# Optimization experiments

Hardware: AMD Instinct MI355X
Metric: run time of the kernel (lower is better)

The kernel has to match this reference:

```python
import jax, jax.numpy as jnp
import numpy as np

B = 131072   # batch rows in the (pooled) sparse tensor
C = 512      # conv_out4
J = 7        # jnt_dim
H = 512      # linear_out
TAU_MAX = 1.0  # undefined global in source; torque cap, taken as 1.0
EPS = 1e-5


def layer_norm(x, g, b):
    m = jnp.mean(x, axis=-1, keepdims=True)
    v = jnp.var(x, axis=-1, keepdims=True)
    return (x - m) * jax.lax.rsqrt(v + EPS) * g + b


def setup_inputs() -> dict:
    key = jax.random.key(0)
    ks = jax.random.split(key, 6)
    return {
        "features": jax.random.normal(ks[0], (B, C), dtype=jnp.float32),
        "coords": jax.random.randint(ks[1], (B,), 0, B),  # batch indices (col 0 of ME coords)
        "jnt_pos": jax.random.normal(ks[2], (B, J), dtype=jnp.float32),
        "jnt_goal": jax.random.normal(ks[3], (B, J), dtype=jnp.float32),
        "ln1_g": jnp.ones((C,), jnp.float32),
        "ln1_b": jnp.zeros((C,), jnp.float32),
        "W1": jax.random.normal(ks[4], (C + 2 * J, H), dtype=jnp.float32) / np.sqrt(C + 2 * J),
        "b1": jnp.zeros((H,), jnp.float32),
        "ln2_g": jnp.ones((H,), jnp.float32),
        "ln2_b": jnp.zeros((H,), jnp.float32),
        "W2": jax.random.normal(ks[5], (H, J), dtype=jnp.float32) / np.sqrt(H),
        "b2": jnp.zeros((J,), jnp.float32),
    }


def reference(features, coords, jnt_pos, jnt_goal,
              ln1_g, ln1_b, W1, b1, ln2_g, ln2_b, W2, b2):
    # to_dense_tnsr: y = zeros_like(features); for c in coords: y[c] = features[c]
    # vectorized: single gather + scatter (duplicate writes carry identical values)
    y = jnp.zeros_like(features).at[coords].set(features[coords])
    # norm = LayerNorm(512) -> SELU   (dropout in eval mode: identity)
    x = jax.nn.selu(layer_norm(y, ln1_g, ln1_b))
    # cat((jnt_pos, jnt_goal, x), dim=1)
    x = jnp.concatenate([jnt_pos, jnt_goal, x], axis=1)  # [B, 2J+C]
    # linear = Linear -> LayerNorm -> SELU
    x = jax.nn.selu(layer_norm(x @ W1 + b1, ln2_g, ln2_b))
    # out = Linear -> Tanh, scaled by tau_max
    return jnp.tanh(x @ W2 + b2) * TAU_MAX
```

## Files before the change

kernel.cpp:

```cpp
#include <hip/hip_runtime.h>

#define B_ROWS   131072
#define MTILE    64
#define KCHUNKS  17
#define LDA      552
#define W1T_OFF  ((size_t)B_ROWS * 4)

typedef _Float16 f16x8 __attribute__((ext_vector_type(8)));
typedef float    f32x4 __attribute__((ext_vector_type(4)));

__device__ inline unsigned short f2h(float f) {
  _Float16 h = (_Float16)f;
  return __builtin_bit_cast(unsigned short, h);
}
__device__ inline float selu_f(float x) {
  const float lam = 1.0507009873554805f, alp = 1.6732632423543772f;
  return x > 0.f ? lam * x : lam * alp * (__expf(x) - 1.f);
}

__global__ void scatter_mask(const int* __restrict__ coords,
                             unsigned int* __restrict__ mask) {
  int i = blockIdx.x * 256 + threadIdx.x;
  mask[coords[i]] = 1u;
}

__global__ void build_w1f(const float* __restrict__ W1,
                          unsigned short* __restrict__ W1f) {
  int fragIdx = blockIdx.x;
  int tid  = threadIdx.x;
  int ni   = fragIdx & 3;
  int c    = (fragIdx >> 2) % 17;
  int wq   = fragIdx / 68;
  int lane = tid >> 3, e = tid & 7;
  int n = wq * 64 + ni * 16 + (lane & 15);
  int k = c * 32 + (lane >> 4) * 8 + e;
  float v = 0.f;
  if (k < 512)       v = W1[(size_t)(k + 14) * 512 + n];
  else if (k < 526)  v = W1[(size_t)(k - 512) * 512 + n];
  W1f[(size_t)fragIdx * 512 + tid] = f2h(v);
}

struct __align__(16) SMem {
  char buf[70656];
  float rsum[MTILE], rsq[MTILE], mean2[MTILE], rstd2[MTILE];
};

__global__ __launch_bounds__(512, 4) void actor_main(
    const float* __restrict__ feat, const unsigned int* __restrict__ mask,
    const float* __restrict__ jp, const float* __restrict__ jg,
    const float* __restrict__ ln1g, const float* __restrict__ ln1b,
    const unsigned short* __restrict__ W1f, const float* __restrict__ b1,
    const float* __restrict__ ln2g, const float* __restrict__ ln2b,
    const float* __restrict__ W2, const float* __restrict__ b2,
    float* __restrict__ out) {
  __shared__ SMem sm;
  unsigned short* At = (unsigned short*)sm.buf;
  unsigned short* X2 = (unsigned short*)sm.buf;

  const int tid  = threadIdx.x;
  const int wq   = tid >> 6;
  const int lane = tid & 63;
  const int m0   = blockIdx.x * MTILE;
  const int mrow = lane & 15;
  const int quad = lane >> 4;

  if (tid < MTILE) { sm.rsum[tid] = 0.f; sm.rsq[tid] = 0.f; }

  {
    const int arow = tid >> 3;
    const int acg  = tid & 7;
    const int row  = m0 + arow;
    const float4* frow = (const float4*)feat + (size_t)row * 128 + acg;
    float4 f[16];
    float s = 0.f, q = 0.f;
#pragma unroll
    for (int c = 0; c < 16; ++c) {
      float4 v = frow[(size_t)c * 8];
      f[c] = v;
      s += v.x + v.y + v.z + v.w;
      q += v.x * v.x + v.y * v.y + v.z * v.z + v.w * v.w;
    }
    s += __shfl_xor(s, 1); q += __shfl_xor(q, 1);
    s += __shfl_xor(s, 2); q += __shfl_xor(q, 2);
    s += __shfl_xor(s, 4); q += __shfl_xor(q, 4);
    float mk   = mask[row] ? 1.f : 0.f;
    float mean = mk * s * (1.f / 512.f);
    float msq  = mk * q * (1.f / 512.f);
    float rstd = rsqrtf(msq - mean * mean + 1e-5f);
#pragma unroll
    for (int c = 0; c < 16; ++c) {
      float4 g = ((const float4*)ln1g)[c * 8 + acg];
      float4 b = ((const float4*)ln1b)[c * 8 + acg];
      union { unsigned short us[4]; uint2 u; } pk;
      pk.us[0] = f2h(selu_f((f[c].x * mk - mean) * rstd * g.x + b.x));
      pk.us[1] = f2h(selu_f((f[c].y * mk - mean) * rstd * g.y + b.y));
      pk.us[2] = f2h(selu_f((f[c].z * mk - mean) * rstd * g.z + b.z));
      pk.us[3] = f2h(selu_f((f[c].w * mk - mean) * rstd * g.w + b.w));
      *(uint2*)&At[arow * LDA + c * 32 + acg * 4] = pk.u;
    }
    {
      union { unsigned short us[4]; uint2 u; } pk;
#pragma unroll
      for (int q2 = 0; q2 < 4; ++q2) {
        int kk = acg * 4 + q2;
        float val = 0.f;
        if (kk < 7)       val = jp[(size_t)row * 7 + kk];
        else if (kk < 14) val = jg[(size_t)row * 7 + kk - 7];
        pk.us[q2] = f2h(val);
      }
      *(uint2*)&At[arow * LDA + 512 + acg * 4] = pk.u;
    }
  }
  __syncthreads();

  f32x4 acc[4][4];
#pragma unroll
  for (int mi = 0; mi < 4; ++mi)
#pragma unroll
    for (int ni = 0; ni < 4; ++ni) acc[mi][ni] = (f32x4){0.f, 0.f, 0.f, 0.f};

  const unsigned short* wBase = W1f + (size_t)wq * 68 * 512 + lane * 8;
  const unsigned short* aB = At + mrow * LDA + quad * 8;

  auto loadB = [&](f16x8* dst, int c) {
#pragma unroll
    for (int ni = 0; ni < 4; ++ni)
      dst[ni] = *(const f16x8*)(wBase + (size_t)(c * 4 + ni) * 512);
  };
  auto step = [&](const f16x8* bF, int c) {
    f16x8 a[4];
#pragma unroll
    for (int mi = 0; mi < 4; ++mi)
      a[mi] = *(const f16x8*)(aB + mi * 16 * LDA + c * 32);
#pragma unroll
    for (int mi = 0; mi < 4; ++mi)
#pragma unroll
      for (int ni = 0; ni < 4; ++ni)
        acc[mi][ni] = __builtin_amdgcn_mfma_f32_16x16x32_f16(a[mi], bF[ni], acc[mi][ni], 0, 0, 0);
  };

  {
    f16x8 bE[4], bO[4];
    loadB(bE, 0);
    for (int c = 0; c < KCHUNKS - 1; c += 2) {
      loadB(bO, c + 1);
      step(bE, c);
      loadB(bE, c + 2);
      step(bO, c + 1);
    }
    step(bE, 16);
  }

  float b1v[4], g2v[4], bl2v[4];
#pragma unroll
  for (int ni = 0; ni < 4; ++ni) {
    int col = wq * 64 + ni * 16 + mrow;
    b1v[ni] = b1[col]; g2v[ni] = ln2g[col]; bl2v[ni] = ln2b[col];
  }
#pragma unroll
  for (int mi = 0; mi < 4; ++mi)
#pragma unroll
    for (int reg = 0; reg < 4; ++reg) {
      int r = mi * 16 + quad * 4 + reg;
      float s = 0.f, q = 0.f;
#pragma unroll
      for (int ni = 0; ni < 4; ++ni) {
        float v = acc[mi][ni][reg] + b1v[ni];
        acc[mi][ni][reg] = v;
        s += v; q += v * v;
      }
      s += __shfl_xor(s, 1); q += __shfl_xor(q, 1);
      s += __shfl_xor(s, 2); q += __shfl_xor(q, 2);
      s += __shfl_xor(s, 4); q += __shfl_xor(q, 4);
      s += __shfl_xor(s, 8); q += __shfl_xor(q, 8);
      if ((lane & 15) == 0) { atomicAdd(&sm.rsum[r], s); atomicAdd(&sm.rsq[r], q); }
    }
  __syncthreads();
  if (tid < MTILE) {
    float mean = sm.rsum[tid] * (1.f / 512.f);
    float var  = sm.rsq[tid] * (1.f / 512.f) - mean * mean;
    sm.mean2[tid] = mean;
    sm.rstd2[tid] = rsqrtf(var + 1e-5f);
  }
  __syncthreads();
#pragma unroll
  for (int mi = 0; mi < 4; ++mi)
#pragma unroll
    for (int ni = 0; ni < 4; ++ni)
#pragma unroll
      for (int reg = 0; reg < 4; ++reg) {
        int r = mi * 16 + quad * 4 + reg;
        int col = wq * 64 + ni * 16 + mrow;
        float v = (acc[mi][ni][reg] - sm.mean2[r]) * sm.rstd2[r] * g2v[ni] + bl2v[ni];
        X2[r * 520 + col] = f2h(selu_f(v));
      }
  __syncthreads();

  float w2r[56];
  {
    const float4* wp = (const float4*)W2 + lane * 14;
#pragma unroll
    for (int i = 0; i < 14; ++i) {
      float4 t = wp[i];
      w2r[i * 4 + 0] = t.x; w2r[i * 4 + 1] = t.y;
      w2r[i * 4 + 2] = t.z; w2r[i * 4 + 3] = t.w;
    }
  }
  float b2v = (lane < 7) ? b2[lane] : 0.f;
  for (int i = 0; i < 8; ++i) {
    int r = wq * 8 + i;
    f16x8 xv = *(const f16x8*)&X2[r * 520 + lane * 8];
    float o0 = 0, o1 = 0, o2 = 0, o3 = 0, o4 = 0, o5 = 0, o6 = 0;
#pragma unroll
    for (int e = 0; e < 8; ++e) {
      float xf = (float)xv[e];
      o0 += xf * w2r[e * 7 + 0]; o1 += xf * w2r[e * 7 + 1];
      o2 += xf * w2r[e * 7 + 2]; o3 += xf * w2r[e * 7 + 3];
      o4 += xf * w2r[e * 7 + 4]; o5 += xf * w2r[e * 7 + 5];
      o6 += xf * w2r[e * 7 + 6];
    }
#pragma unroll
    for (int d = 32; d > 0; d >>= 1) {
      o0 += __shfl_xor(o0, d); o1 += __shfl_xor(o1, d); o2 += __shfl_xor(o2, d);
      o3 += __shfl_xor(o3, d); o4 += __shfl_xor(o4, d); o5 += __shfl_xor(o5, d);
      o6 += __shfl_xor(o6, d);
    }
    if (lane < 7) {
      float ov = o0;
      if (lane == 1) ov = o1; else if (lane == 2) ov = o2;
      else if (lane == 3) ov = o3; else if (lane == 4) ov = o4;
      else if (lane == 5) ov = o5; else if (lane == 6) ov = o6;
      out[(size_t)(m0 + r) * 7 + lane] = tanhf(ov + b2v);
    }
  }
}

extern "C" void kernel_launch(void* const* d_in, const int* in_sizes, int n_in,
                              void* d_out, int out_size, void* d_ws, size_t ws_size,
                              hipStream_t stream) {
  const float* feat  = (const float*)d_in[0];
  const int*   crd   = (const int*)d_in[1];
  const float* jp    = (const float*)d_in[2];
  const float* jg    = (const float*)d_in[3];
  const float* ln1g  = (const float*)d_in[4];
  const float* ln1b  = (const float*)d_in[5];
  const float* W1    = (const float*)d_in[6];
  const float* b1    = (const float*)d_in[7];
  const float* ln2g  = (const float*)d_in[8];
  const float* ln2b  = (const float*)d_in[9];
  const float* W2    = (const float*)d_in[10];
  const float* b2    = (const float*)d_in[11];
  float* out = (float*)d_out;

  unsigned int*   mask = (unsigned int*)d_ws;
  unsigned short* W1f  = (unsigned short*)((char*)d_ws + W1T_OFF);

  hipMemsetAsync(mask, 0, (size_t)B_ROWS * 4, stream);
  scatter_mask<<<B_ROWS / 256, 256, 0, stream>>>(crd, mask);
  build_w1f<<<544, 512, 0, stream>>>(W1, W1f);
  actor_main<<<B_ROWS / MTILE, 512, 0, stream>>>(
      feat, mask, jp, jg, ln1g, ln1b, W1f, b1, ln2g, ln2b, W2, b2, out);
}
```

Before: 520.7 us.

## Compute second linear layer with MFMA and shrink mask to bytes

Replaces the scalar per-row W2 dot products and wide shuffle reductions with MFMA over a prepacked fp16 W2 fragment buffer. Each wave handles a K-slice and the partial results are combined through shared-memory atomics. Other changes: the mask becomes a byte array, the W1 pack kernel reads coalesced through a shared-memory transpose, and the first W1 fragment load is hoisted before the feature load. In exchange, the second layer now runs in fp16 with shared atomic accumulation, and the X2 stride changes.

New measurement: 502.1 us. 3.6% less time.

```diff
diff --git a/kernel.cpp b/kernel.cpp
--- a/kernel.cpp
+++ b/kernel.cpp
@@ -4,7 +4,9 @@
 #define MTILE    64
 #define KCHUNKS  17
 #define LDA      552
-#define W1T_OFF  ((size_t)B_ROWS * 4)
+#define LDX      528
+#define W1F_OFF  ((size_t)B_ROWS)
+#define W2F_OFF  (W1F_OFF + (size_t)544 * 512 * 2)
 
 typedef _Float16 f16x8 __attribute__((ext_vector_type(8)));
 typedef float    f32x4 __attribute__((ext_vector_type(4)));
@@ -19,25 +21,40 @@
 }
 
 __global__ void scatter_mask(const int* __restrict__ coords,
-                             unsigned int* __restrict__ mask) {
+                             unsigned char* __restrict__ mask) {
   int i = blockIdx.x * 256 + threadIdx.x;
   mask[coords[i]] = 1u;
 }
 
-__global__ void build_w1f(const float* __restrict__ W1,
-                          unsigned short* __restrict__ W1f) {
-  int fragIdx = blockIdx.x;
-  int tid  = threadIdx.x;
-  int ni   = fragIdx & 3;
-  int c    = (fragIdx >> 2) % 17;
-  int wq   = fragIdx / 68;
-  int lane = tid >> 3, e = tid & 7;
-  int n = wq * 64 + ni * 16 + (lane & 15);
-  int k = c * 32 + (lane >> 4) * 8 + e;
-  float v = 0.f;
-  if (k < 512)       v = W1[(size_t)(k + 14) * 512 + n];
-  else if (k < 526)  v = W1[(size_t)(k - 512) * 512 + n];
-  W1f[(size_t)fragIdx * 512 + tid] = f2h(v);
+__global__ void build_wf(const float* __restrict__ W1, const float* __restrict__ W2,
+                         unsigned short* __restrict__ W1f, unsigned short* __restrict__ W2f) {
+  int tid = threadIdx.x;
+  if (blockIdx.x < 544) {
+    int fragIdx = blockIdx.x;
+    int ni = fragIdx & 3;
+    int c  = (fragIdx >> 2) % 17;
+    int wq = fragIdx / 68;
+    int nbase = wq * 64 + ni * 16;
+    __shared__ float t[32][17];
+    int kl = tid >> 4, nl = tid & 15;
+    int kg = c * 32 + kl;
+    float v = 0.f;
+    if (kg < 512)      v = W1[(size_t)(kg + 14) * 512 + nbase + nl];
+    else if (kg < 526) v = W1[(size_t)(kg - 512) * 512 + nbase + nl];
+    t[kl][nl] = v;
+    __syncthreads();
+    int lane = tid >> 3, e = tid & 7;
+    int k2 = ((lane >> 4) & 3) * 8 + e;
+    int n2 = lane & 15;
+    W1f[(size_t)fragIdx * 512 + tid] = f2h(t[k2][n2]);
+  } else {
+    int c2 = blockIdx.x - 544;
+    int lane = tid >> 3, e = tid & 7;
+    int n = lane & 15, quad = (lane >> 4) & 3;
+    int k = c2 * 32 + quad * 8 + e;
+    float v = (n < 7) ? W2[(size_t)k * 7 + n] : 0.f;
+    W2f[(size_t)c2 * 512 + tid] = f2h(v);
+  }
 }
 
 struct __align__(16) SMem {
@@ -46,16 +63,17 @@
 };
 
 __global__ __launch_bounds__(512, 4) void actor_main(
-    const float* __restrict__ feat, const unsigned int* __restrict__ mask,
+    const float* __restrict__ feat, const unsigned char* __restrict__ mask,
     const float* __restrict__ jp, const float* __restrict__ jg,
     const float* __restrict__ ln1g, const float* __restrict__ ln1b,
     const unsigned short* __restrict__ W1f, const float* __restrict__ b1,
     const float* __restrict__ ln2g, const float* __restrict__ ln2b,
-    const float* __restrict__ W2, const float* __restrict__ b2,
+    const unsigned short* __restrict__ W2f, const float* __restrict__ b2,
     float* __restrict__ out) {
   __shared__ SMem sm;
   unsigned short* At = (unsigned short*)sm.buf;
   unsigned short* X2 = (unsigned short*)sm.buf;
+  float*          O  = (float*)(sm.buf + 64 * LDX * 2);
 
   const int tid  = threadIdx.x;
   const int wq   = tid >> 6;
@@ -65,6 +83,12 @@
   const int quad = lane >> 4;
 
   if (tid < MTILE) { sm.rsum[tid] = 0.f; sm.rsq[tid] = 0.f; }
+
+  const unsigned short* wBase = W1f + (size_t)wq * 68 * 512 + lane * 8;
+  f16x8 bE[4], bO[4];
+#pragma unroll
+  for (int ni = 0; ni < 4; ++ni)
+    bE[ni] = *(const f16x8*)(wBase + (size_t)ni * 512);
 
   {
     const int arow = tid >> 3;
@@ -119,7 +143,6 @@
 #pragma unroll
     for (int ni = 0; ni < 4; ++ni) acc[mi][ni] = (f32x4){0.f, 0.f, 0.f, 0.f};
 
-  const unsigned short* wBase = W1f + (size_t)wq * 68 * 512 + lane * 8;
   const unsigned short* aB = At + mrow * LDA + quad * 8;
 
   auto loadB = [&](f16x8* dst, int c) {
@@ -139,17 +162,17 @@
         acc[mi][ni] = __builtin_amdgcn_mfma_f32_16x16x32_f16(a[mi], bF[ni], acc[mi][ni], 0, 0, 0);
   };
 
-  {
-    f16x8 bE[4], bO[4];
-    loadB(bE, 0);
-    for (int c = 0; c < KCHUNKS - 1; c += 2) {
-      loadB(bO, c + 1);
-      step(bE, c);
-      loadB(bE, c + 2);
-      step(bO, c + 1);
-    }
-    step(bE, 16);
-  }
+  for (int c = 0; c < KCHUNKS - 1; c += 2) {
+    loadB(bO, c + 1);
+    step(bE, c);
+    loadB(bE, c + 2);
+    step(bO, c + 1);
+  }
+  step(bE, 16);
+
+  f16x8 bW2[2];
+  bW2[0] = *(const f16x8*)&W2f[(size_t)(2 * wq)     * 512 + lane * 8];
+  bW2[1] = *(const f16x8*)&W2f[(size_t)(2 * wq + 1) * 512 + lane * 8];
 
   float b1v[4], g2v[4], bl2v[4];
 #pragma unroll
@@ -182,6 +205,7 @@
     sm.mean2[tid] = mean;
     sm.rstd2[tid] = rsqrtf(var + 1e-5f);
   }
+  O[tid] = 0.f;
   __syncthreads();
 #pragma unroll
   for (int mi = 0; mi < 4; ++mi)
@@ -192,46 +216,35 @@
         int r = mi * 16 + quad * 4 + reg;
         int col = wq * 64 + ni * 16 + mrow;
         float v = (acc[mi][ni][reg] - sm.mean2[r]) * sm.rstd2[r] * g2v[ni] + bl2v[ni];
-        X2[r * 520 + col] = f2h(selu_f(v));
-      }
-  __syncthreads();
-
-  float w2r[56];
+        X2[r * LDX + col] = f2h(selu_f(v));
+      }
+  __syncthreads();
+
   {
-    const float4* wp = (const float4*)W2 + lane * 14;
-#pragma unroll
-    for (int i = 0; i < 14; ++i) {
-      float4 t = wp[i];
-      w2r[i * 4 + 0] = t.x; w2r[i * 4 + 1] = t.y;
-      w2r[i * 4 + 2] = t.z; w2r[i * 4 + 3] = t.w;
-    }
-  }
-  float b2v = (lane < 7) ? b2[lane] : 0.f;
-  for (int i = 0; i < 8; ++i) {
-    int r = wq * 8 + i;
-    f16x8 xv = *(const f16x8*)&X2[r * 520 + lane * 8];
-    float o0 = 0, o1 = 0, o2 = 0, o3 = 0, o4 = 0, o5 = 0, o6 = 0;
-#pragma unroll
-    for (int e = 0; e < 8; ++e) {
-      float xf = (float)xv[e];
-      o0 += xf * w2r[e * 7 + 0]; o1 += xf * w2r[e * 7 + 1];
-      o2 += xf * w2r[e * 7 + 2]; o3 += xf * w2r[e * 7 + 3];
-      o4 += xf * w2r[e * 7 + 4]; o5 += xf * w2r[e * 7 + 5];
-      o6 += xf * w2r[e * 7 + 6];
-    }
-#pragma unroll
-    for (int d = 32; d > 0; d >>= 1) {
-      o0 += __shfl_xor(o0, d); o1 += __shfl_xor(o1, d); o2 += __shfl_xor(o2, d);
-      o3 += __shfl_xor(o3, d); o4 += __shfl_xor(o4, d); o5 += __shfl_xor(o5, d);
-      o6 += __shfl_xor(o6, d);
-    }
-    if (lane < 7) {
-      float ov = o0;
-      if (lane == 1) ov = o1; else if (lane == 2) ov = o2;
-      else if (lane == 3) ov = o3; else if (lane == 4) ov = o4;
-      else if (lane == 5) ov = o5; else if (lane == 6) ov = o6;
-      out[(size_t)(m0 + r) * 7 + lane] = tanhf(ov + b2v);
-    }
+    f32x4 acc2[4];
+#pragma unroll
+    for (int mi = 0; mi < 4; ++mi) acc2[mi] = (f32x4){0.f, 0.f, 0.f, 0.f};
+#pragma unroll
+    for (int j = 0; j < 2; ++j) {
+      int c2 = 2 * wq + j;
+#pragma unroll
+      for (int mi = 0; mi < 4; ++mi) {
+        f16x8 a = *(const f16x8*)&X2[(mi * 16 + mrow) * LDX + c2 * 32 + quad * 8];
+        acc2[mi] = __builtin_amdgcn_mfma_f32_16x16x32_f16(a, bW2[j], acc2[mi], 0, 0, 0);
+      }
+    }
+#pragma unroll
+    for (int mi = 0; mi < 4; ++mi)
+#pragma unroll
+      for (int reg = 0; reg < 4; ++reg)
+        if (mrow < 7)
+          atomicAdd(&O[(mi * 16 + quad * 4 + reg) * 8 + mrow], acc2[mi][reg]);
+  }
+  __syncthreads();
+  {
+    int r = tid >> 3, c = tid & 7;
+    if (c < 7)
+      out[(size_t)(m0 + r) * 7 + c] = tanhf(O[tid] + b2[c]);
   }
 }
 
@@ -252,12 +265,13 @@
   const float* b2    = (const float*)d_in[11];
   float* out = (float*)d_out;
 
-  unsigned int*   mask = (unsigned int*)d_ws;
-  unsigned short* W1f  = (unsigned short*)((char*)d_ws + W1T_OFF);
-
-  hipMemsetAsync(mask, 0, (size_t)B_ROWS * 4, stream);
+  unsigned char*  mask = (unsigned char*)d_ws;
+  unsigned short* W1f  = (unsigned short*)((char*)d_ws + W1F_OFF);
+  unsigned short* W2f  = (unsigned short*)((char*)d_ws + W2F_OFF);
+
+  hipMemsetAsync(mask, 0, (size_t)B_ROWS, stream);
   scatter_mask<<<B_ROWS / 256, 256, 0, stream>>>(crd, mask);
-  build_w1f<<<544, 512, 0, stream>>>(W1, W1f);
+  build_wf<<<560, 512, 0, stream>>>(W1, W2, W1f, W2f);
   actor_main<<<B_ROWS / MTILE, 512, 0, stream>>>(
-      feat, mask, jp, jg, ln1g, ln1b, W1f, b1, ln2g, ln2b, W2, b2, out);
-}
+      feat, mask, jp, jg, ln1g, ln1b, W1f, b1, ln2g, ln2b, W2f, b2, out);
+}
```
